# Optimization experiments

Hardware: AMD Instinct MI355X
Metric: run time of the kernel (lower is better)

## Reference

```python
import jax, jax.numpy as jnp
import numpy as np

LEN_HIS = 20   # q_len_his: sliding-window history length
DIM_C = 4      # dim_c
H = 64         # GRU hidden = final_mlp_hidden_width
D = 36         # global_graph_width(32) + goal(2) + action(2)
N = 32768      # total timesteps across many episodes


def setup_inputs() -> dict:
    key = jax.random.key(0)
    ks = jax.random.split(key, 8)
    emb = jax.random.normal(ks[0], (N, D), jnp.float32)
    dones = (jax.random.uniform(ks[1], (N, 1)) < 0.02).astype(jnp.int32)
    s = lambda k, shape, fan: jax.random.normal(k, shape, jnp.float32) / np.sqrt(fan).astype(np.float32)
    return {
        "embeddings": emb,
        "W_ih": s(ks[2], (3 * H, D), D),
        "W_hh": s(ks[3], (3 * H, H), H),
        "b_ih": jnp.zeros((3 * H,), jnp.float32),
        "b_hh": jnp.zeros((3 * H,), jnp.float32),
        "W1": s(ks[4], (H, H), H),
        "b1": jnp.zeros((H,), jnp.float32),
        "W2": s(ks[5], (DIM_C, H), H),
        "b2": jnp.zeros((DIM_C,), jnp.float32),
        "dones": dones,
    }


def _his_calculate_c(embeddings, W_ih, W_hh, b_ih, b_hh, W1, b1, W2, b2, dones):
    """Batched/padded version of the ragged sliding-window GRU+MLP loop.

    For each timestep t, the torch code runs the GRU over
    embeddings[max(episode_start, t-L+1) : t+1] from a zero hidden state,
    then applies FinalPredMLP to the final hidden state.
    """
    n = embeddings.shape[0]
    done = dones[:, 0] != 0
    idx = jnp.arange(n)
    # episode_start[t] = (index of most recent done strictly before t) + 1, else 0
    prev_done = jnp.concatenate([jnp.zeros((1,), bool), done[:-1]])
    ep_start = jax.lax.cummax(jnp.where(prev_done, idx, 0))
    win_start = jnp.maximum(ep_start, idx - LEN_HIS + 1)            # [N]

    # padded windows: position l holds embeddings[t - (L-1) + l]
    gidx = idx[:, None] - (LEN_HIS - 1) + jnp.arange(LEN_HIS)[None, :]  # [N, L]
    valid = gidx >= win_start[:, None]                                   # [N, L]
    X = embeddings[jnp.clip(gidx, 0, n - 1)] * valid[..., None]          # [N, L, D]

    def cell(h, inp):
        x, v = inp                      # x: [N, D], v: [N]
        gi = x @ W_ih.T + b_ih          # [N, 3H]
        gh = h @ W_hh.T + b_hh          # [N, 3H]
        ir, iz, inn = jnp.split(gi, 3, axis=-1)
        hr, hz, hnn = jnp.split(gh, 3, axis=-1)
        r = jax.nn.sigmoid(ir + hr)
        z = jax.nn.sigmoid(iz + hz)
        ncand = jnp.tanh(inn + r * hnn)
        h_new = (1.0 - z) * ncand + z * h
        return jnp.where(v[:, None], h_new, h), None

    h0 = jnp.zeros((n, H), embeddings.dtype)
    hT, _ = jax.lax.scan(cell, h0, (jnp.swapaxes(X, 0, 1), valid.T))  # [N, H]

    # FinalPredMLP: Linear(H,H) -> ReLU -> Linear(H, dim_c)
    hid = jax.nn.relu(hT @ W1.T + b1)
    return hid @ W2.T + b2              # [N, dim_c]


def reference(embeddings, W_ih, W_hh, b_ih, b_hh, W1, b1, W2, b2, dones):
    return _his_calculate_c(embeddings, W_ih, W_hh, b_ih, b_hh, W1, b1, W2, b2, dones)
```

## Files before the change

kernel.cpp:

```cpp
#include <hip/hip_runtime.h>

#define NT 32768
#define DI 36
#define HH 64
#define LH 20
#define TPB 64
#define NROW 83
#define SGS 196
#define EMBS 40

#define NLOG2E -1.4426950408889634f
#define TLOG2E 2.8853900817779268f

#define UNION_OFF  65072
#define SMEM_BYTES 78608

typedef __attribute__((ext_vector_type(8))) short bf16x8;
typedef __attribute__((ext_vector_type(4))) float f32x4;
typedef __attribute__((ext_vector_type(4))) int int4v;
union frag_cast { int4v i4; bf16x8 h8; };

__device__ __forceinline__ unsigned f2u(float f) { union { float f; unsigned u; } x; x.f = f; return x.u; }
__device__ __forceinline__ float u2f(unsigned u) { union { float f; unsigned u; } x; x.u = u; return x.f; }
__device__ __forceinline__ unsigned short f2bf_rne(float f) {
    union { float f; unsigned u; } x; x.f = f;
    unsigned r = x.u + 0x7FFFu + ((x.u >> 16) & 1u);
    return (unsigned short)(r >> 16);
}

__device__ __forceinline__ void gate4(const f32x4 aR, const f32x4 aZ,
                                      const f32x4 aI, const f32x4 aN,
                                      const bool valid, float* hh) {
    float dR[4], dZ[4], dN[4], rv[4], zv[4], iv[4];
#pragma unroll
    for (int e = 0; e < 4; ++e) dR[e] = 1.f + __builtin_amdgcn_exp2f(aR[e]);
#pragma unroll
    for (int e = 0; e < 4; ++e) dZ[e] = 1.f + __builtin_amdgcn_exp2f(aZ[e]);
    {
        const float pa = dR[0] * dR[1], pb = dR[2] * dR[3];
        const float rp = __builtin_amdgcn_rcpf(pa * pb);
        const float ia = rp * pb, ib = rp * pa;
        rv[0] = ia * dR[1]; rv[1] = ia * dR[0];
        rv[2] = ib * dR[3]; rv[3] = ib * dR[2];
    }
    {
        const float pa = dZ[0] * dZ[1], pb = dZ[2] * dZ[3];
        const float rp = __builtin_amdgcn_rcpf(pa * pb);
        const float ia = rp * pb, ib = rp * pa;
        zv[0] = ia * dZ[1]; zv[1] = ia * dZ[0];
        zv[2] = ib * dZ[3]; zv[3] = ib * dZ[2];
    }
#pragma unroll
    for (int e = 0; e < 4; ++e)
        dN[e] = 1.f + __builtin_amdgcn_exp2f(fmaf(rv[e], aN[e], aI[e]));
    {
        const float pa = dN[0] * dN[1], pb = dN[2] * dN[3];
        const float rp = __builtin_amdgcn_rcpf(pa * pb);
        const float ia = rp * pb, ib = rp * pa;
        iv[0] = ia * dN[1]; iv[1] = ia * dN[0];
        iv[2] = ib * dN[3]; iv[3] = ib * dN[2];
    }
#pragma unroll
    for (int e = 0; e < 4; ++e) {
        const float nc = fmaf(-2.f, iv[e], 1.f);
        const float hn = fmaf(zv[e], hh[e] - nc, nc);
        hh[e] = valid ? hn : hh[e];
    }
}

__global__ __launch_bounds__(64) void prep_kernel(
    const float* __restrict__ W_ih, const float* __restrict__ W_hh,
    const float* __restrict__ W1, int4v* __restrict__ wfrag)
{
    const int b = (int)blockIdx.x;
    const int l = (int)threadIdx.x;
    unsigned short e[8];
    if (b < 72) {
        const int set = b / 24, fb = b % 24;
        const int mt = fb >> 1, kt = fb & 1;
        const int m = mt * 16 + (l & 15);
        const float sc = ((mt >> 2) < 2) ? NLOG2E : TLOG2E;
        const int k0 = kt * 32 + (l >> 4) * 8;
#pragma unroll
        for (int jj = 0; jj < 8; ++jj) {
            const int k = k0 + jj;
            if (set == 2) {
                e[jj] = f2bf_rne(W_hh[(size_t)m * HH + k] * sc);
            } else {
                const float v = (k < DI) ? W_ih[(size_t)m * DI + k] * sc : 0.f;
                const unsigned u = f2u(v);
                if (set == 0) e[jj] = (unsigned short)(u >> 16);
                else          e[jj] = (unsigned short)(f2u(v - u2f(u & 0xFFFF0000u)) >> 16);
            }
        }
    } else {
        const int bb = b - 72;
        const bool is_lo = bb >= 8;
        const int f = bb & 7;
        const int mt = f >> 1, kt = f & 1;
        const int m = mt * 16 + (l & 15);
        const int k0 = kt * 32 + (l >> 4) * 8;
#pragma unroll
        for (int jj = 0; jj < 8; ++jj) {
            const float v = W1[(size_t)m * HH + k0 + jj];
            const unsigned u = f2u(v);
            if (!is_lo) e[jj] = (unsigned short)(u >> 16);
            else        e[jj] = (unsigned short)(f2u(v - u2f(u & 0xFFFF0000u)) >> 16);
        }
    }
    int4v p;
    p.x = e[0] | ((unsigned)e[1] << 16); p.y = e[2] | ((unsigned)e[3] << 16);
    p.z = e[4] | ((unsigned)e[5] << 16); p.w = e[6] | ((unsigned)e[7] << 16);
    wfrag[b * 64 + l] = p;
}

__global__ __launch_bounds__(256, 2) void gru_kernel(
    const float* __restrict__ emb, const int4v* __restrict__ wfrag,
    const float* __restrict__ b_ih, const float* __restrict__ b_hh,
    const float* __restrict__ b1, const float* __restrict__ W2,
    const float* __restrict__ b2, const int* __restrict__ dones,
    float* __restrict__ out)
{
    __shared__ __align__(16) char SMEM[SMEM_BYTES];
    float* const Sg = (float*)SMEM;
    unsigned short* const EmbH = (unsigned short*)(SMEM + UNION_OFF);
    unsigned short* const EmbL = EmbH + NROW * EMBS;
    unsigned short* const Hb   = (unsigned short*)(SMEM + UNION_OFF);

    const int tid = threadIdx.x;
    const int lane = tid & 63;
    const int W = tid >> 6;
    const int li = lane & 15;
    const int q = lane >> 4;
    const int blk = ((int)blockIdx.x & 7) * 64 + ((int)blockIdx.x >> 3);
    const int T0 = blk * TPB;

    int sfr;
    {
        const int tt = T0 + 16 * W + li;
        int off = (tt >= LH - 1) ? 0 : (LH - 1) - tt;
#pragma unroll
        for (int k = LH - 1; k >= 1; --k) {
            const int j = tt - k;
            const int jj = j < 0 ? 0 : j;
            const bool d = (j >= 0) && (dones[jj] != 0);
            if (d) off = LH - k;
        }
        sfr = off;
    }

    for (int i = tid; i < NROW * 9; i += 256) {
        const int r = i / 9, c = i - r * 9;
        int tt = T0 - (LH - 1) + r; tt = tt < 0 ? 0 : tt;
        const f32x4 v = *(const f32x4*)&emb[(size_t)tt * DI + 4 * c];
        const unsigned u0 = f2u(v[0]), u1 = f2u(v[1]);
        const unsigned u2 = f2u(v[2]), u3 = f2u(v[3]);
        uint2 ph, pl;
        ph.x = __builtin_amdgcn_perm(u1, u0, 0x07060302u);
        ph.y = __builtin_amdgcn_perm(u3, u2, 0x07060302u);
        const unsigned l0 = f2u(v[0] - u2f(u0 & 0xFFFF0000u));
        const unsigned l1 = f2u(v[1] - u2f(u1 & 0xFFFF0000u));
        const unsigned l2 = f2u(v[2] - u2f(u2 & 0xFFFF0000u));
        const unsigned l3 = f2u(v[3] - u2f(u3 & 0xFFFF0000u));
        pl.x = __builtin_amdgcn_perm(l1, l0, 0x07060302u);
        pl.y = __builtin_amdgcn_perm(l3, l2, 0x07060302u);
        *(uint2*)&EmbH[r * EMBS + 4 * c] = ph;
        *(uint2*)&EmbL[r * EMBS + 4 * c] = pl;
    }
    if (tid < NROW) {
        const uint2 z2 = {0u, 0u};
        *(uint2*)&EmbH[tid * EMBS + DI] = z2;
        *(uint2*)&EmbL[tid * EMBS + DI] = z2;
    }

    bf16x8 aih[3][2], ail[3][2];
#pragma unroll
    for (int g = 0; g < 3; ++g)
#pragma unroll
        for (int kt = 0; kt < 2; ++kt) {
            const int fb = (4 * g + W) * 2 + kt;
            frag_cast a, b;
            a.i4 = wfrag[(0 * 24 + fb) * 64 + lane];
            b.i4 = wfrag[(1 * 24 + fb) * 64 + lane];
            aih[g][kt] = a.h8; ail[g][kt] = b.h8;
        }
    bf16x8 whh[3][4][2];
#pragma unroll
    for (int g = 0; g < 3; ++g)
#pragma unroll
        for (int mt = 0; mt < 4; ++mt)
#pragma unroll
            for (int kt = 0; kt < 2; ++kt) {
                frag_cast c;
                c.i4 = wfrag[(48 + (4 * g + mt) * 2 + kt) * 64 + lane];
                whh[g][mt][kt] = c.h8;
            }

    const int joff = 16 * W + 4 * q;
    f32x4 biasI[3];
#pragma unroll
    for (int g = 0; g < 3; ++g) {
        const float sc = (g < 2) ? NLOG2E : TLOG2E;
        const f32x4 bi = *(const f32x4*)&b_ih[64 * g + joff];
        if (g < 2) {
            const f32x4 bh = *(const f32x4*)&b_hh[64 * g + joff];
#pragma unroll
            for (int rr = 0; rr < 4; ++rr) biasI[g][rr] = (bi[rr] + bh[rr]) * sc;
        } else {
#pragma unroll
            for (int rr = 0; rr < 4; ++rr) biasI[g][rr] = bi[rr] * sc;
        }
    }
    __syncthreads();

#pragma unroll
    for (int rt = 0; rt < 6; ++rt) {
        const int row0 = (rt == 5) ? 67 : 16 * rt;
        const int row = row0 + li;
        bf16x8 ebh0 = *(const bf16x8*)&EmbH[row * EMBS + 8 * q];
        bf16x8 ebl0 = *(const bf16x8*)&EmbL[row * EMBS + 8 * q];
        bf16x8 ebh1 = bf16x8{0, 0, 0, 0, 0, 0, 0, 0};
        bf16x8 ebl1 = bf16x8{0, 0, 0, 0, 0, 0, 0, 0};
        if (q == 0) {
            ebh1 = *(const bf16x8*)&EmbH[row * EMBS + 32];
            ebl1 = *(const bf16x8*)&EmbL[row * EMBS + 32];
        }
#pragma unroll
        for (int g = 0; g < 3; ++g) {
            f32x4 a = biasI[g];
            a = __builtin_amdgcn_mfma_f32_16x16x32_bf16(aih[g][0], ebh0, a, 0, 0, 0);
            a = __builtin_amdgcn_mfma_f32_16x16x32_bf16(aih[g][1], ebh1, a, 0, 0, 0);
            a = __builtin_amdgcn_mfma_f32_16x16x32_bf16(ail[g][0], ebh0, a, 0, 0, 0);
            a = __builtin_amdgcn_mfma_f32_16x16x32_bf16(ail[g][1], ebh1, a, 0, 0, 0);
            a = __builtin_amdgcn_mfma_f32_16x16x32_bf16(aih[g][0], ebl0, a, 0, 0, 0);
            a = __builtin_amdgcn_mfma_f32_16x16x32_bf16(aih[g][1], ebl1, a, 0, 0, 0);
            *(f32x4*)&Sg[row * SGS + 64 * g + joff] = a;
        }
    }
    __syncthreads();

    f32x4 bnv4[4];
#pragma unroll
    for (int mt = 0; mt < 4; ++mt) {
        const f32x4 b = *(const f32x4*)&b_hh[128 + 16 * mt + 4 * q];
#pragma unroll
        for (int rr = 0; rr < 4; ++rr) bnv4[mt][rr] = b[rr] * TLOG2E;
    }
    unsigned short* const Hbw = Hb + W * 1152;

    float h[4][4];
    f32x4 gvR[4], gvZ[4], gvI[4];
    bf16x8 bh0, bh1;
    {
        const float* gp = Sg + (16 * W + li) * SGS;
        const bool valid = (0 >= sfr);
#pragma unroll
        for (int mt = 0; mt < 4; ++mt) {
            const f32x4 aR = *(const f32x4*)(gp + 16 * mt + 4 * q);
            const f32x4 aZ = *(const f32x4*)(gp + 64 + 16 * mt + 4 * q);
            const f32x4 aI = *(const f32x4*)(gp + 128 + 16 * mt + 4 * q);
            h[mt][0] = 0.f; h[mt][1] = 0.f; h[mt][2] = 0.f; h[mt][3] = 0.f;
            gate4(aR, aZ, aI, bnv4[mt], valid, h[mt]);
            uint2 ph;
            ph.x = __builtin_amdgcn_perm(f2u(h[mt][1]), f2u(h[mt][0]), 0x07060302u);
            ph.y = __builtin_amdgcn_perm(f2u(h[mt][3]), f2u(h[mt][2]), 0x07060302u);
            *(uint2*)&Hbw[li * 72 + 16 * mt + 4 * q] = ph;
        }
        bh0 = *(const bf16x8*)&Hbw[li * 72 + 8 * q];
        bh1 = *(const bf16x8*)&Hbw[li * 72 + 32 + 8 * q];
        const float* gq = Sg + (16 * W + li + 1) * SGS;
#pragma unroll
        for (int mt = 0; mt < 4; ++mt) {
            gvR[mt] = *(const f32x4*)(gq + 16 * mt + 4 * q);
            gvZ[mt] = *(const f32x4*)(gq + 64 + 16 * mt + 4 * q);
            gvI[mt] = *(const f32x4*)(gq + 128 + 16 * mt + 4 * q);
        }
    }

#pragma unroll 2
    for (int s = 1; s < LH; ++s) {
        const bool last = (s == LH - 1);
        f32x4 aR[4], aZ[4], aN[4], aI[4];
#pragma unroll
        for (int mt = 0; mt < 4; ++mt) {
            aR[mt] = gvR[mt]; aZ[mt] = gvZ[mt]; aI[mt] = gvI[mt]; aN[mt] = bnv4[mt];
        }
        {
            int rrow = 16 * W + li + s + 1; rrow = rrow > NROW - 1 ? NROW - 1 : rrow;
            const float* gq = Sg + rrow * SGS;
#pragma unroll
            for (int mt = 0; mt < 4; ++mt) {
                gvR[mt] = *(const f32x4*)(gq + 16 * mt + 4 * q);
                gvZ[mt] = *(const f32x4*)(gq + 64 + 16 * mt + 4 * q);
                gvI[mt] = *(const f32x4*)(gq + 128 + 16 * mt + 4 * q);
            }
        }
#pragma unroll
        for (int mt = 0; mt < 4; ++mt) {
            aR[mt] = __builtin_amdgcn_mfma_f32_16x16x32_bf16(whh[0][mt][0], bh0, aR[mt], 0, 0, 0);
            aR[mt] = __builtin_amdgcn_mfma_f32_16x16x32_bf16(whh[0][mt][1], bh1, aR[mt], 0, 0, 0);
            aZ[mt] = __builtin_amdgcn_mfma_f32_16x16x32_bf16(whh[1][mt][0], bh0, aZ[mt], 0, 0, 0);
            aZ[mt] = __builtin_amdgcn_mfma_f32_16x16x32_bf16(whh[1][mt][1], bh1, aZ[mt], 0, 0, 0);
            aN[mt] = __builtin_amdgcn_mfma_f32_16x16x32_bf16(whh[2][mt][0], bh0, aN[mt], 0, 0, 0);
            aN[mt] = __builtin_amdgcn_mfma_f32_16x16x32_bf16(whh[2][mt][1], bh1, aN[mt], 0, 0, 0);
        }
        const bool valid = (s >= sfr);
#pragma unroll
        for (int mt = 0; mt < 2; ++mt) {
            gate4(aR[mt], aZ[mt], aI[mt], aN[mt], valid, h[mt]);
            if (!last) {
                uint2 ph;
                ph.x = __builtin_amdgcn_perm(f2u(h[mt][1]), f2u(h[mt][0]), 0x07060302u);
                ph.y = __builtin_amdgcn_perm(f2u(h[mt][3]), f2u(h[mt][2]), 0x07060302u);
                *(uint2*)&Hbw[li * 72 + 16 * mt + 4 * q] = ph;
            }
        }
        if (!last) bh0 = *(const bf16x8*)&Hbw[li * 72 + 8 * q];
#pragma unroll
        for (int mt = 2; mt < 4; ++mt) {
            gate4(aR[mt], aZ[mt], aI[mt], aN[mt], valid, h[mt]);
            if (!last) {
                uint2 ph;
                ph.x = __builtin_amdgcn_perm(f2u(h[mt][1]), f2u(h[mt][0]), 0x07060302u);
                ph.y = __builtin_amdgcn_perm(f2u(h[mt][3]), f2u(h[mt][2]), 0x07060302u);
                *(uint2*)&Hbw[li * 72 + 16 * mt + 4 * q] = ph;
            }
        }
        if (!last) bh1 = *(const bf16x8*)&Hbw[li * 72 + 32 + 8 * q];
    }

    bf16x8 w1h[4][2], w1l[4][2];
#pragma unroll
    for (int mt = 0; mt < 4; ++mt)
#pragma unroll
        for (int kt = 0; kt < 2; ++kt) {
            frag_cast a, b;
            a.i4 = wfrag[(72 + mt * 2 + kt) * 64 + lane];
            b.i4 = wfrag[(80 + mt * 2 + kt) * 64 + lane];
            w1h[mt][kt] = a.h8; w1l[mt][kt] = b.h8;
        }
#pragma unroll
    for (int mt = 0; mt < 4; ++mt) {
        uint2 ph;
        ph.x = __builtin_amdgcn_perm(f2u(h[mt][1]), f2u(h[mt][0]), 0x07060302u);
        ph.y = __builtin_amdgcn_perm(f2u(h[mt][3]), f2u(h[mt][2]), 0x07060302u);
        *(uint2*)&Hbw[li * 72 + 16 * mt + 4 * q] = ph;
    }
    const bf16x8 fh0 = *(const bf16x8*)&Hbw[li * 72 + 8 * q];
    const bf16x8 fh1 = *(const bf16x8*)&Hbw[li * 72 + 32 + 8 * q];
#pragma unroll
    for (int mt = 0; mt < 4; ++mt) {
        const unsigned u0 = f2u(h[mt][0]), u1 = f2u(h[mt][1]);
        const unsigned u2 = f2u(h[mt][2]), u3 = f2u(h[mt][3]);
        const unsigned l0 = f2u(h[mt][0] - u2f(u0 & 0xFFFF0000u));
        const unsigned l1 = f2u(h[mt][1] - u2f(u1 & 0xFFFF0000u));
        const unsigned l2 = f2u(h[mt][2] - u2f(u2 & 0xFFFF0000u));
        const unsigned l3 = f2u(h[mt][3] - u2f(u3 & 0xFFFF0000u));
        uint2 pl;
        pl.x = __builtin_amdgcn_perm(l1, l0, 0x07060302u);
        pl.y = __builtin_amdgcn_perm(l3, l2, 0x07060302u);
        *(uint2*)&Hbw[li * 72 + 16 * mt + 4 * q] = pl;
    }
    const bf16x8 fl0 = *(const bf16x8*)&Hbw[li * 72 + 8 * q];
    const bf16x8 fl1 = *(const bf16x8*)&Hbw[li * 72 + 32 + 8 * q];

    float p0 = 0.f, p1 = 0.f, p2 = 0.f, p3 = 0.f;
#pragma unroll
    for (int mt = 0; mt < 4; ++mt) {
        f32x4 a = *(const f32x4*)&b1[16 * mt + 4 * q];
        a = __builtin_amdgcn_mfma_f32_16x16x32_bf16(w1h[mt][0], fh0, a, 0, 0, 0);
        a = __builtin_amdgcn_mfma_f32_16x16x32_bf16(w1h[mt][1], fh1, a, 0, 0, 0);
        a = __builtin_amdgcn_mfma_f32_16x16x32_bf16(w1l[mt][0], fh0, a, 0, 0, 0);
        a = __builtin_amdgcn_mfma_f32_16x16x32_bf16(w1l[mt][1], fh1, a, 0, 0, 0);
        a = __builtin_amdgcn_mfma_f32_16x16x32_bf16(w1h[mt][0], fl0, a, 0, 0, 0);
        a = __builtin_amdgcn_mfma_f32_16x16x32_bf16(w1h[mt][1], fl1, a, 0, 0, 0);
        const float h0 = fmaxf(a[0], 0.f), h1 = fmaxf(a[1], 0.f);
        const float h2 = fmaxf(a[2], 0.f), h3 = fmaxf(a[3], 0.f);
        const f32x4 w0 = *(const f32x4*)&W2[0 * HH + 16 * mt + 4 * q];
        const f32x4 w1 = *(const f32x4*)&W2[1 * HH + 16 * mt + 4 * q];
        const f32x4 w2 = *(const f32x4*)&W2[2 * HH + 16 * mt + 4 * q];
        const f32x4 w3 = *(const f32x4*)&W2[3 * HH + 16 * mt + 4 * q];
        p0 += h0 * w0[0] + h1 * w0[1] + h2 * w0[2] + h3 * w0[3];
        p1 += h0 * w1[0] + h1 * w1[1] + h2 * w1[2] + h3 * w1[3];
        p2 += h0 * w2[0] + h1 * w2[1] + h2 * w2[2] + h3 * w2[3];
        p3 += h0 * w3[0] + h1 * w3[1] + h2 * w3[2] + h3 * w3[3];
    }
    p0 += __shfl_xor(p0, 16); p0 += __shfl_xor(p0, 32);
    p1 += __shfl_xor(p1, 16); p1 += __shfl_xor(p1, 32);
    p2 += __shfl_xor(p2, 16); p2 += __shfl_xor(p2, 32);
    p3 += __shfl_xor(p3, 16); p3 += __shfl_xor(p3, 32);
    const float pv = (q == 0) ? p0 : (q == 1) ? p1 : (q == 2) ? p2 : p3;
    out[(size_t)(T0 + 16 * W + li) * 4 + q] = pv + b2[q];
}

extern "C" void kernel_launch(void* const* d_in, const int* in_sizes, int n_in,
                              void* d_out, int out_size, void* d_ws, size_t ws_size,
                              hipStream_t stream) {
    const float* emb  = (const float*)d_in[0];
    const float* W_ih = (const float*)d_in[1];
    const float* W_hh = (const float*)d_in[2];
    const float* b_ih = (const float*)d_in[3];
    const float* b_hh = (const float*)d_in[4];
    const float* W1   = (const float*)d_in[5];
    const float* b1   = (const float*)d_in[6];
    const float* W2   = (const float*)d_in[7];
    const float* b2   = (const float*)d_in[8];
    const int*   dn   = (const int*)d_in[9];

    int4v* wfrag = (int4v*)d_ws;
    float* o = (float*)d_out;

    prep_kernel<<<88, 64, 0, stream>>>(W_ih, W_hh, W1, wfrag);
    gru_kernel<<<NT / TPB, 256, 0, stream>>>(emb, wfrag, b_ih, b_hh,
                                             b1, W2, b2, dn, o);
}
```

Before: 113.4 us.

## Store precomputed input-gate activations in fp16 shared memory to raise occupancy

The per-block table of input projections (x·W_ih + bias, pre-scaled by log2e factors) is packed to fp16 with round-toward-zero instead of kept as fp32, roughly halving its shared-memory footprint and the LDS traffic of the per-step prefetch. The smaller LDS allocation lets the launch bound request three blocks per CU instead of two, aiming for more latency hiding in the serial GRU recurrence. The cost is extra fp16-to-fp32 conversions on every step, and lower precision for gate inputs, which carry exp2 scaling and could lose accuracy. Raising the occupancy target may also constrain the register budget and cause spills.

```diff
diff --git a/kernel.cpp b/kernel.cpp
--- a/kernel.cpp
+++ b/kernel.cpp
@@ -6,19 +6,21 @@
 #define LH 20
 #define TPB 64
 #define NROW 83
-#define SGS 196
+#define SGH 200
 #define EMBS 40
 
 #define NLOG2E -1.4426950408889634f
 #define TLOG2E 2.8853900817779268f
 
-#define UNION_OFF  65072
-#define SMEM_BYTES 78608
+#define UNION_OFF  33200
+#define SMEM_BYTES 46480
 
 typedef __attribute__((ext_vector_type(8))) short bf16x8;
+typedef __attribute__((ext_vector_type(4))) _Float16 f16x4;
 typedef __attribute__((ext_vector_type(4))) float f32x4;
 typedef __attribute__((ext_vector_type(4))) int int4v;
 union frag_cast { int4v i4; bf16x8 h8; };
+union u2h4 { uint2 u; f16x4 h; };
 
 __device__ __forceinline__ unsigned f2u(float f) { union { float f; unsigned u; } x; x.f = f; return x.u; }
 __device__ __forceinline__ float u2f(unsigned u) { union { float f; unsigned u; } x; x.u = u; return x.f; }
@@ -26,6 +28,10 @@
     union { float f; unsigned u; } x; x.f = f;
     unsigned r = x.u + 0x7FFFu + ((x.u >> 16) & 1u);
     return (unsigned short)(r >> 16);
+}
+__device__ __forceinline__ unsigned pk2h(float a, float b) {
+    auto h = __builtin_amdgcn_cvt_pkrtz(a, b);
+    union { decltype(h) v; unsigned u; } x; x.v = h; return x.u;
 }
 
 __device__ __forceinline__ void gate4(const f32x4 aR, const f32x4 aZ,
@@ -114,7 +120,7 @@
     wfrag[b * 64 + l] = p;
 }
 
-__global__ __launch_bounds__(256, 2) void gru_kernel(
+__global__ __launch_bounds__(256, 3) void gru_kernel(
     const float* __restrict__ emb, const int4v* __restrict__ wfrag,
     const float* __restrict__ b_ih, const float* __restrict__ b_hh,
     const float* __restrict__ b1, const float* __restrict__ W2,
@@ -122,7 +128,7 @@
     float* __restrict__ out)
 {
     __shared__ __align__(16) char SMEM[SMEM_BYTES];
-    float* const Sg = (float*)SMEM;
+    unsigned short* const Sgh  = (unsigned short*)SMEM;
     unsigned short* const EmbH = (unsigned short*)(SMEM + UNION_OFF);
     unsigned short* const EmbL = EmbH + NROW * EMBS;
     unsigned short* const Hb   = (unsigned short*)(SMEM + UNION_OFF);
@@ -234,7 +240,10 @@
             a = __builtin_amdgcn_mfma_f32_16x16x32_bf16(ail[g][1], ebh1, a, 0, 0, 0);
             a = __builtin_amdgcn_mfma_f32_16x16x32_bf16(aih[g][0], ebl0, a, 0, 0, 0);
             a = __builtin_amdgcn_mfma_f32_16x16x32_bf16(aih[g][1], ebl1, a, 0, 0, 0);
-            *(f32x4*)&Sg[row * SGS + 64 * g + joff] = a;
+            uint2 pk;
+            pk.x = pk2h(a[0], a[1]);
+            pk.y = pk2h(a[2], a[3]);
+            *(uint2*)&Sgh[row * SGH + 64 * g + joff] = pk;
         }
     }
     __syncthreads();
@@ -249,16 +258,22 @@
     unsigned short* const Hbw = Hb + W * 1152;
 
     float h[4][4];
-    f32x4 gvR[4], gvZ[4], gvI[4];
+    uint2 gvR[4], gvZ[4], gvI[4];
     bf16x8 bh0, bh1;
     {
-        const float* gp = Sg + (16 * W + li) * SGS;
+        const int gp = (16 * W + li) * SGH;
         const bool valid = (0 >= sfr);
 #pragma unroll
         for (int mt = 0; mt < 4; ++mt) {
-            const f32x4 aR = *(const f32x4*)(gp + 16 * mt + 4 * q);
-            const f32x4 aZ = *(const f32x4*)(gp + 64 + 16 * mt + 4 * q);
-            const f32x4 aI = *(const f32x4*)(gp + 128 + 16 * mt + 4 * q);
+            u2h4 cR, cZ, cI;
+            cR.u = *(const uint2*)&Sgh[gp + 16 * mt + 4 * q];
+            cZ.u = *(const uint2*)&Sgh[gp + 64 + 16 * mt + 4 * q];
+            cI.u = *(const uint2*)&Sgh[gp + 128 + 16 * mt + 4 * q];
+            f32x4 aR, aZ, aI;
+#pragma unroll
+            for (int rr = 0; rr < 4; ++rr) {
+                aR[rr] = (float)cR.h[rr]; aZ[rr] = (float)cZ.h[rr]; aI[rr] = (float)cI.h[rr];
+            }
             h[mt][0] = 0.f; h[mt][1] = 0.f; h[mt][2] = 0.f; h[mt][3] = 0.f;
             gate4(aR, aZ, aI, bnv4[mt], valid, h[mt]);
             uint2 ph;
@@ -268,12 +283,12 @@
         }
         bh0 = *(const bf16x8*)&Hbw[li * 72 + 8 * q];
         bh1 = *(const bf16x8*)&Hbw[li * 72 + 32 + 8 * q];
-        const float* gq = Sg + (16 * W + li + 1) * SGS;
+        const int gq = (16 * W + li + 1) * SGH;
 #pragma unroll
         for (int mt = 0; mt < 4; ++mt) {
-            gvR[mt] = *(const f32x4*)(gq + 16 * mt + 4 * q);
-            gvZ[mt] = *(const f32x4*)(gq + 64 + 16 * mt + 4 * q);
-            gvI[mt] = *(const f32x4*)(gq + 128 + 16 * mt + 4 * q);
+            gvR[mt] = *(const uint2*)&Sgh[gq + 16 * mt + 4 * q];
+            gvZ[mt] = *(const uint2*)&Sgh[gq + 64 + 16 * mt + 4 * q];
+            gvI[mt] = *(const uint2*)&Sgh[gq + 128 + 16 * mt + 4 * q];
         }
     }
 
@@ -283,16 +298,24 @@
         f32x4 aR[4], aZ[4], aN[4], aI[4];
 #pragma unroll
         for (int mt = 0; mt < 4; ++mt) {
-            aR[mt] = gvR[mt]; aZ[mt] = gvZ[mt]; aI[mt] = gvI[mt]; aN[mt] = bnv4[mt];
+            u2h4 cR, cZ, cI;
+            cR.u = gvR[mt]; cZ.u = gvZ[mt]; cI.u = gvI[mt];
+#pragma unroll
+            for (int rr = 0; rr < 4; ++rr) {
+                aR[mt][rr] = (float)cR.h[rr];
+                aZ[mt][rr] = (float)cZ.h[rr];
+                aI[mt][rr] = (float)cI.h[rr];
+            }
+            aN[mt] = bnv4[mt];
         }
         {
             int rrow = 16 * W + li + s + 1; rrow = rrow > NROW - 1 ? NROW - 1 : rrow;
-            const float* gq = Sg + rrow * SGS;
+            const int gq = rrow * SGH;
 #pragma unroll
             for (int mt = 0; mt < 4; ++mt) {
-                gvR[mt] = *(const f32x4*)(gq + 16 * mt + 4 * q);
-                gvZ[mt] = *(const f32x4*)(gq + 64 + 16 * mt + 4 * q);
-                gvI[mt] = *(const f32x4*)(gq + 128 + 16 * mt + 4 * q);
+                gvR[mt] = *(const uint2*)&Sgh[gq + 16 * mt + 4 * q];
+                gvZ[mt] = *(const uint2*)&Sgh[gq + 64 + 16 * mt + 4 * q];
+                gvI[mt] = *(const uint2*)&Sgh[gq + 128 + 16 * mt + 4 * q];
             }
         }
 #pragma unroll
```

Measured after the change: 161.1 us. +42.1%, slower.
